# Kernel optimization log

Hardware: AMD Instinct MI355X
Metric: run time of the kernel (lower is better)

The kernel has to match this reference:

```python
import jax, jax.numpy as jnp
import numpy as np

B, IN_FEATURES, OUT_FEATURES, NUM_CONN, K_OPS = 512, 4096, 4096, 64, 4


def setup_inputs() -> dict:
    key = jax.random.key(0)
    k1, k2, k3 = jax.random.split(key, 3)
    x = jax.random.normal(k1, (B, IN_FEATURES), dtype=jnp.float32)
    # per-output random fan-in connections (randperm(in)[:num_conn] in original)
    connection_indices = jax.random.randint(k2, (OUT_FEATURES, NUM_CONN), 0, IN_FEATURES, dtype=jnp.int32)
    # per-output choice among the K aggregation operators
    operator_table_indices = jax.random.randint(k3, (OUT_FEATURES,), 0, K_OPS, dtype=jnp.int32)
    return {"x": x, "connection_indices": connection_indices,
            "operator_table_indices": operator_table_indices}


def reference(x, connection_indices, operator_table_indices):
    # gather: [B, out_features, num_connections]
    features = x[:, connection_indices]
    # operator_table = [mean, sum, amax, amin], each reducing dim=2
    # stacked along axis=1 -> output: [B, K, out_features]
    output = jnp.stack([
        features.mean(axis=2),
        features.sum(axis=2),
        features.max(axis=2),
        features.min(axis=2),
    ], axis=1)
    # select chosen operator per output unit -> fwd: [B, out_features]
    idx = operator_table_indices[None, None, :]  # [1,1,O] broadcast over batch
    fwd = jnp.take_along_axis(output, idx, axis=1)[:, 0, :]
    return (fwd, output)
```

## Files before the change

### kernel.cpp

```cpp
#include <hip/hip_runtime.h>

#define IN_F   4096
#define OUT_F  4096
#define BATCH  512
#define NCONN  64
#define BT     4
#define OGRP   1024
#define NTHR   1024

typedef _Float16 h4v __attribute__((ext_vector_type(4)));

__global__ __launch_bounds__(256) void connT_kernel(const int* __restrict__ conn,
                                                    int* __restrict__ connT) {
    __shared__ int tile[64][65];
    const int o0 = blockIdx.x * 64;
    const int tx = threadIdx.x & 63;
    const int ty = threadIdx.x >> 6;
#pragma unroll
    for (int r = 0; r < 16; ++r) {
        const int row = ty * 16 + r;
        tile[row][tx] = conn[(size_t)(o0 + row) * NCONN + tx];
    }
    __syncthreads();
#pragma unroll
    for (int r = 0; r < 16; ++r) {
        const int k = ty * 16 + r;
        connT[(size_t)k * OUT_F + o0 + tx] = tile[tx][k];
    }
}

__global__ __launch_bounds__(NTHR, 8) void agg_kernel(const float* __restrict__ x,
                                                      const int* __restrict__ connT,
                                                      const int* __restrict__ opidx,
                                                      float* __restrict__ out) {
    __shared__ alignas(16) _Float16 xs[IN_F * BT];

    const int bid   = blockIdx.x;
    const int btile = (bid & 7) * 16 + (bid >> 5);
    const int og    = (bid >> 3) & 3;
    const int o0    = og * OGRP;
    const int b0    = btile * BT;
    const int t     = threadIdx.x;

    const int bb   = t & 3;
    const int joff = t >> 2;
    const float* __restrict__ xrow = x + (size_t)(b0 + bb) * IN_F;
#pragma unroll 4
    for (int it = 0; it < 16; ++it) {
        const int j = it * 256 + joff;
        xs[j * BT + bb] = (_Float16)xrow[j];
    }
    __syncthreads();

    const int o = o0 + t;
    const int* __restrict__ cp = connT + o;

    float s0 = 0.f, s1 = 0.f, s2 = 0.f, s3 = 0.f;
    float mx0 = -__builtin_inff(), mx1 = mx0, mx2 = mx0, mx3 = mx0;
    float mn0 =  __builtin_inff(), mn1 = mn0, mn2 = mn0, mn3 = mn0;

    int idx[8];
#pragma unroll
    for (int q = 0; q < 8; ++q) idx[q] = cp[(size_t)q * OUT_F];

    for (int kb = 0; kb < NCONN; kb += 8) {
        h4v v[8];
#pragma unroll
        for (int q = 0; q < 8; ++q)
            v[q] = *reinterpret_cast<const h4v*>(&xs[idx[q] * BT]);
        if (kb + 8 < NCONN) {
#pragma unroll
            for (int q = 0; q < 8; ++q) idx[q] = cp[(size_t)(kb + 8 + q) * OUT_F];
        }
#pragma unroll
        for (int q = 0; q < 8; ++q) {
            const float f0 = (float)v[q][0];
            const float f1 = (float)v[q][1];
            const float f2 = (float)v[q][2];
            const float f3 = (float)v[q][3];
            s0 += f0;  s1 += f1;  s2 += f2;  s3 += f3;
            mx0 = fmaxf(mx0, f0); mx1 = fmaxf(mx1, f1);
            mx2 = fmaxf(mx2, f2); mx3 = fmaxf(mx3, f3);
            mn0 = fminf(mn0, f0); mn1 = fminf(mn1, f1);
            mn2 = fminf(mn2, f2); mn3 = fminf(mn3, f3);
        }
    }

    const int op = opidx[o];
    float* __restrict__ fwd  = out;
    float* __restrict__ outp = out + (size_t)BATCH * OUT_F;

    const float sv[4] = {s0, s1, s2, s3};
    const float xv[4] = {mx0, mx1, mx2, mx3};
    const float nv[4] = {mn0, mn1, mn2, mn3};
#pragma unroll
    for (int i = 0; i < 4; ++i) {
        const float ss = sv[i];
        const float mm = ss * 0.015625f;
        const float hx = xv[i];
        const float ln = nv[i];
        const float fw = (op == 0) ? mm : (op == 1) ? ss : (op == 2) ? hx : ln;
        const size_t rowO = (size_t)(b0 + i) * (4 * OUT_F) + o;
        __builtin_nontemporal_store(fw, fwd + (size_t)(b0 + i) * OUT_F + o);
        __builtin_nontemporal_store(mm, outp + rowO);
        __builtin_nontemporal_store(ss, outp + rowO + OUT_F);
        __builtin_nontemporal_store(hx, outp + rowO + 2 * OUT_F);
        __builtin_nontemporal_store(ln, outp + rowO + 3 * OUT_F);
    }
}

extern "C" void kernel_launch(void* const* d_in, const int* in_sizes, int n_in,
                              void* d_out, int out_size, void* d_ws, size_t ws_size,
                              hipStream_t stream) {
    const float* x     = (const float*)d_in[0];
    const int*   conn  = (const int*)d_in[1];
    const int*   opidx = (const int*)d_in[2];
    float*       out   = (float*)d_out;
    int*         connT = (int*)d_ws;

    connT_kernel<<<OUT_F / 64, 256, 0, stream>>>(conn, connT);

    const int nblocks = (BATCH / BT) * (OUT_F / OGRP);
    agg_kernel<<<nblocks, NTHR, 0, stream>>>(x, connT, opidx, out);
}
```

Before: 27.97 us.

## Pack connection indices as u16x4 and do max/min in packed half precision

The preprocessing kernel now packs connection indices into 16-bit values grouped four per 8-byte vector. The aggregation kernel can then load four indices per global access, with a two-stage register prefetch. Max and min are now computed on packed fp16 vectors instead of after converting each element to fp32, which cuts VALU work; sums stay in fp32. This relies on IN_F fitting in 16 bits. Max/min results are unchanged, since the inputs were already rounded to fp16.

```diff
diff --git a/kernel.cpp b/kernel.cpp
--- a/kernel.cpp
+++ b/kernel.cpp
@@ -8,29 +8,56 @@
 #define OGRP   1024
 #define NTHR   1024
 
+typedef unsigned short u16;
+typedef u16 us4 __attribute__((ext_vector_type(4)));
 typedef _Float16 h4v __attribute__((ext_vector_type(4)));
 
-__global__ __launch_bounds__(256) void connT_kernel(const int* __restrict__ conn,
-                                                    int* __restrict__ connT) {
-    __shared__ int tile[64][65];
+static __device__ __forceinline__ h4v h4_max(h4v a, h4v b) {
+    h4v r;
+#pragma unroll
+    for (int i = 0; i < 4; ++i) r[i] = a[i] > b[i] ? a[i] : b[i];
+    return r;
+}
+static __device__ __forceinline__ h4v h4_min(h4v a, h4v b) {
+    h4v r;
+#pragma unroll
+    for (int i = 0; i < 4; ++i) r[i] = a[i] < b[i] ? a[i] : b[i];
+    return r;
+}
+
+__global__ __launch_bounds__(256) void pack_kernel(const int* __restrict__ conn,
+                                                   us4* __restrict__ connP) {
+    __shared__ u16 tile[64][68];
     const int o0 = blockIdx.x * 64;
-    const int tx = threadIdx.x & 63;
-    const int ty = threadIdx.x >> 6;
+    const int t  = threadIdx.x;
+    const int ol = t >> 2;
+    const int4* __restrict__ c4 = reinterpret_cast<const int4*>(conn);
 #pragma unroll
-    for (int r = 0; r < 16; ++r) {
-        const int row = ty * 16 + r;
-        tile[row][tx] = conn[(size_t)(o0 + row) * NCONN + tx];
+    for (int i = 0; i < 4; ++i) {
+        const int4 v = c4[(size_t)(o0 + ol) * 16 + (t & 3) * 4 + i];
+        const int kbase = (t & 3) * 16 + i * 4;
+        tile[ol][kbase + 0] = (u16)v.x;
+        tile[ol][kbase + 1] = (u16)v.y;
+        tile[ol][kbase + 2] = (u16)v.z;
+        tile[ol][kbase + 3] = (u16)v.w;
     }
     __syncthreads();
+    const int o  = o0 + (t & 63);
+    const int k0 = (t >> 6) * 4;
 #pragma unroll
-    for (int r = 0; r < 16; ++r) {
-        const int k = ty * 16 + r;
-        connT[(size_t)k * OUT_F + o0 + tx] = tile[tx][k];
+    for (int i = 0; i < 4; ++i) {
+        const int kb = k0 + i;
+        us4 p;
+        p[0] = tile[t & 63][4 * kb + 0];
+        p[1] = tile[t & 63][4 * kb + 1];
+        p[2] = tile[t & 63][4 * kb + 2];
+        p[3] = tile[t & 63][4 * kb + 3];
+        connP[(size_t)kb * OUT_F + o] = p;
     }
 }
 
 __global__ __launch_bounds__(NTHR, 8) void agg_kernel(const float* __restrict__ x,
-                                                      const int* __restrict__ connT,
+                                                      const us4* __restrict__ connP,
                                                       const int* __restrict__ opidx,
                                                       float* __restrict__ out) {
     __shared__ alignas(16) _Float16 xs[IN_F * BT];
@@ -53,59 +80,67 @@
     __syncthreads();
 
     const int o = o0 + t;
-    const int* __restrict__ cp = connT + o;
+    const us4* __restrict__ cp = connP + o;
+
+    us4 i0 = cp[0];
+    us4 i1 = cp[OUT_F];
+    us4 i2 = cp[2 * (size_t)OUT_F];
+    us4 i3 = cp[3 * (size_t)OUT_F];
 
     float s0 = 0.f, s1 = 0.f, s2 = 0.f, s3 = 0.f;
-    float mx0 = -__builtin_inff(), mx1 = mx0, mx2 = mx0, mx3 = mx0;
-    float mn0 =  __builtin_inff(), mn1 = mn0, mn2 = mn0, mn3 = mn0;
+    const _Float16 HNEG = __builtin_bit_cast(_Float16, (u16)0xFC00);
+    const _Float16 HPOS = __builtin_bit_cast(_Float16, (u16)0x7C00);
+    h4v hx = {HNEG, HNEG, HNEG, HNEG};
+    h4v hn = {HPOS, HPOS, HPOS, HPOS};
 
-    int idx[8];
-#pragma unroll
-    for (int q = 0; q < 8; ++q) idx[q] = cp[(size_t)q * OUT_F];
+    const h4v* __restrict__ xs4 = reinterpret_cast<const h4v*>(xs);
 
-    for (int kb = 0; kb < NCONN; kb += 8) {
-        h4v v[8];
-#pragma unroll
-        for (int q = 0; q < 8; ++q)
-            v[q] = *reinterpret_cast<const h4v*>(&xs[idx[q] * BT]);
-        if (kb + 8 < NCONN) {
-#pragma unroll
-            for (int q = 0; q < 8; ++q) idx[q] = cp[(size_t)(kb + 8 + q) * OUT_F];
+    for (int kb = 0; kb < 16; kb += 2) {
+        h4v g[8];
+        g[0] = xs4[i0[0]];  g[1] = xs4[i0[1]];
+        g[2] = xs4[i0[2]];  g[3] = xs4[i0[3]];
+        g[4] = xs4[i1[0]];  g[5] = xs4[i1[1]];
+        g[6] = xs4[i1[2]];  g[7] = xs4[i1[3]];
+
+        us4 inA = i2, inB = i3;
+        if (kb < 12) {
+            inA = cp[(size_t)(kb + 4) * OUT_F];
+            inB = cp[(size_t)(kb + 5) * OUT_F];
         }
+
 #pragma unroll
         for (int q = 0; q < 8; ++q) {
-            const float f0 = (float)v[q][0];
-            const float f1 = (float)v[q][1];
-            const float f2 = (float)v[q][2];
-            const float f3 = (float)v[q][3];
-            s0 += f0;  s1 += f1;  s2 += f2;  s3 += f3;
-            mx0 = fmaxf(mx0, f0); mx1 = fmaxf(mx1, f1);
-            mx2 = fmaxf(mx2, f2); mx3 = fmaxf(mx3, f3);
-            mn0 = fminf(mn0, f0); mn1 = fminf(mn1, f1);
-            mn2 = fminf(mn2, f2); mn3 = fminf(mn3, f3);
+            hx = h4_max(hx, g[q]);
+            hn = h4_min(hn, g[q]);
+            s0 += (float)g[q][0];
+            s1 += (float)g[q][1];
+            s2 += (float)g[q][2];
+            s3 += (float)g[q][3];
         }
+        i0 = i2; i1 = i3; i2 = inA; i3 = inB;
     }
+
+    const float sv[4] = {s0, s1, s2, s3};
+    const float xv[4] = {(float)hx[0], (float)hx[1], (float)hx[2], (float)hx[3]};
+    const float nv[4] = {(float)hn[0], (float)hn[1], (float)hn[2], (float)hn[3]};
 
     const int op = opidx[o];
     float* __restrict__ fwd  = out;
     float* __restrict__ outp = out + (size_t)BATCH * OUT_F;
 
-    const float sv[4] = {s0, s1, s2, s3};
-    const float xv[4] = {mx0, mx1, mx2, mx3};
-    const float nv[4] = {mn0, mn1, mn2, mn3};
 #pragma unroll
     for (int i = 0; i < 4; ++i) {
         const float ss = sv[i];
         const float mm = ss * 0.015625f;
-        const float hx = xv[i];
-        const float ln = nv[i];
-        const float fw = (op == 0) ? mm : (op == 1) ? ss : (op == 2) ? hx : ln;
+        const float hxv = xv[i];
+        const float lnv = nv[i];
+        const float fw = (op == 0) ? mm : (op == 1) ? ss : (op == 2) ? hxv : lnv;
         const size_t rowO = (size_t)(b0 + i) * (4 * OUT_F) + o;
         __builtin_nontemporal_store(fw, fwd + (size_t)(b0 + i) * OUT_F + o);
         __builtin_nontemporal_store(mm, outp + rowO);
         __builtin_nontemporal_store(ss, outp + rowO + OUT_F);
-        __builtin_nontemporal_store(hx, outp + rowO + 2 * OUT_F);
-        __builtin_nontemporal_store(ln, outp + rowO + 3 * OUT_F);
+        __builtin_nontemporal_store(hxv, outp + rowO + 2 * OUT_F);
+        __builtin_nontemporal_store(lnv, outp + rowO + 3 * OUT_F);
     }
 }
 
@@ -116,10 +151,10 @@
     const int*   conn  = (const int*)d_in[1];
     const int*   opidx = (const int*)d_in[2];
     float*       out   = (float*)d_out;
-    int*         connT = (int*)d_ws;
+    us4*         connP = (us4*)d_ws;
 
-    connT_kernel<<<OUT_F / 64, 256, 0, stream>>>(conn, connT);
+    pack_kernel<<<OUT_F / 64, 256, 0, stream>>>(conn, connP);
 
     const int nblocks = (BATCH / BT) * (OUT_F / OGRP);
-    agg_kernel<<<nblocks, NTHR, 0, stream>>>(x, connT, opidx, out);
+    agg_kernel<<<nblocks, NTHR, 0, stream>>>(x, connP, opidx, out);
 }
```

New measurement: 38.44 us. +37.5%, slower.

## Split gathers between LDS and a transposed fp16 global copy, packed half min/max

Applied to the files above, without the earlier changes.

Adds a transpose kernel that writes x as a [IN_F, BATCH] fp16 array, so each gather of four batch values becomes one 8-byte global load. In the aggregation kernel, alternating wavefronts take half of their 64 connections from the LDS tile and half from this global copy, in opposite order, to spread the load between the LDS and the vector memory path. Max and min now run as packed fp16 vector operations instead of scalar fp32. The cost is an extra kernel launch and a full pass over x, more global traffic, and some added code complexity.

```diff
diff --git a/kernel.cpp b/kernel.cpp
--- a/kernel.cpp
+++ b/kernel.cpp
@@ -8,7 +8,39 @@
 #define OGRP   1024
 #define NTHR   1024
 
+typedef unsigned short u16;
 typedef _Float16 h4v __attribute__((ext_vector_type(4)));
+
+__global__ __launch_bounds__(256) void transpose_kernel(const float* __restrict__ x,
+                                                        _Float16* __restrict__ xTh) {
+    __shared__ float tile[64 * 68];
+    const int j0 = blockIdx.x * 64;
+    const int b0 = blockIdx.y * 64;
+    const int t  = threadIdx.x;
+    const int c  = t & 15;
+    const int r0 = t >> 4;
+#pragma unroll
+    for (int it = 0; it < 4; ++it) {
+        const int r  = r0 + it * 16;
+        const int pc = (4 * c) ^ (((r >> 2) & 7) << 2);
+        const float4 v = *reinterpret_cast<const float4*>(
+            x + (size_t)(b0 + r) * IN_F + j0 + 4 * c);
+        *reinterpret_cast<float4*>(&tile[r * 68 + pc]) = v;
+    }
+    __syncthreads();
+#pragma unroll
+    for (int it = 0; it < 4; ++it) {
+        const int jj = r0 + it * 16;
+        h4v v;
+#pragma unroll
+        for (int i = 0; i < 4; ++i) {
+            const int rr   = 4 * c + i;
+            const int pcol = jj ^ (((rr >> 2) & 7) << 2);
+            v[i] = (_Float16)tile[rr * 68 + pcol];
+        }
+        *reinterpret_cast<h4v*>(xTh + (size_t)(j0 + jj) * BATCH + b0 + 4 * c) = v;
+    }
+}
 
 __global__ __launch_bounds__(256) void connT_kernel(const int* __restrict__ conn,
                                                     int* __restrict__ connT) {
@@ -30,6 +62,7 @@
 }
 
 __global__ __launch_bounds__(NTHR, 8) void agg_kernel(const float* __restrict__ x,
+                                                      const _Float16* __restrict__ xTh,
                                                       const int* __restrict__ connT,
                                                       const int* __restrict__ opidx,
                                                       float* __restrict__ out) {
@@ -54,58 +87,87 @@
 
     const int o = o0 + t;
     const int* __restrict__ cp = connT + o;
+    const h4v* __restrict__ xs4 = reinterpret_cast<const h4v*>(xs);
+    const h4v* __restrict__ xg  = reinterpret_cast<const h4v*>(xTh) + (b0 >> 2);
 
     float s0 = 0.f, s1 = 0.f, s2 = 0.f, s3 = 0.f;
-    float mx0 = -__builtin_inff(), mx1 = mx0, mx2 = mx0, mx3 = mx0;
-    float mn0 =  __builtin_inff(), mn1 = mn0, mn2 = mn0, mn3 = mn0;
+    const _Float16 HNEG = __builtin_bit_cast(_Float16, (u16)0xFC00);
+    const _Float16 HPOS = __builtin_bit_cast(_Float16, (u16)0x7C00);
+    h4v hx = {HNEG, HNEG, HNEG, HNEG};
+    h4v hn = {HPOS, HPOS, HPOS, HPOS};
 
-    int idx[8];
+#define CONSUME(gq)                                                         \
+    do {                                                                    \
+        hx = __builtin_elementwise_max(hx, (gq));                           \
+        hn = __builtin_elementwise_min(hn, (gq));                           \
+        s0 = fmaf((float)(gq)[0], 1.0f, s0);                                \
+        s1 = fmaf((float)(gq)[1], 1.0f, s1);                                \
+        s2 = fmaf((float)(gq)[2], 1.0f, s2);                                \
+        s3 = fmaf((float)(gq)[3], 1.0f, s3);                                \
+    } while (0)
+
+    auto lds_phase = [&](int k0) {
+        int idx[8];
 #pragma unroll
-    for (int q = 0; q < 8; ++q) idx[q] = cp[(size_t)q * OUT_F];
+        for (int q = 0; q < 8; ++q) idx[q] = cp[(size_t)(k0 + q) * OUT_F];
+        for (int kb = 0; kb < 32; kb += 8) {
+            h4v g[8];
+#pragma unroll
+            for (int q = 0; q < 8; ++q) g[q] = xs4[idx[q]];
+            if (kb + 8 < 32) {
+#pragma unroll
+                for (int q = 0; q < 8; ++q)
+                    idx[q] = cp[(size_t)(k0 + kb + 8 + q) * OUT_F];
+            }
+#pragma unroll
+            for (int q = 0; q < 8; ++q) CONSUME(g[q]);
+        }
+    };
 
-    for (int kb = 0; kb < NCONN; kb += 8) {
-        h4v v[8];
+    auto glob_phase = [&](int k0) {
+        int idx[8];
 #pragma unroll
-        for (int q = 0; q < 8; ++q)
-            v[q] = *reinterpret_cast<const h4v*>(&xs[idx[q] * BT]);
-        if (kb + 8 < NCONN) {
+        for (int q = 0; q < 8; ++q) idx[q] = cp[(size_t)(k0 + q) * OUT_F];
+        for (int kb = 0; kb < 32; kb += 8) {
+            h4v g[8];
 #pragma unroll
-            for (int q = 0; q < 8; ++q) idx[q] = cp[(size_t)(kb + 8 + q) * OUT_F];
+            for (int q = 0; q < 8; ++q)
+                g[q] = xg[(size_t)idx[q] * (BATCH / 4)];
+            if (kb + 8 < 32) {
+#pragma unroll
+                for (int q = 0; q < 8; ++q)
+                    idx[q] = cp[(size_t)(k0 + kb + 8 + q) * OUT_F];
+            }
+#pragma unroll
+            for (int q = 0; q < 8; ++q) CONSUME(g[q]);
         }
-#pragma unroll
-        for (int q = 0; q < 8; ++q) {
-            const float f0 = (float)v[q][0];
-            const float f1 = (float)v[q][1];
-            const float f2 = (float)v[q][2];
-            const float f3 = (float)v[q][3];
-            s0 += f0;  s1 += f1;  s2 += f2;  s3 += f3;
-            mx0 = fmaxf(mx0, f0); mx1 = fmaxf(mx1, f1);
-            mx2 = fmaxf(mx2, f2); mx3 = fmaxf(mx3, f3);
-            mn0 = fminf(mn0, f0); mn1 = fminf(mn1, f1);
-            mn2 = fminf(mn2, f2); mn3 = fminf(mn3, f3);
-        }
-    }
+    };
+
+    if ((t >> 6) & 1) { lds_phase(0);  glob_phase(32); }
+    else              { glob_phase(0); lds_phase(32);  }
+#undef CONSUME
+
+    const float sv[4] = {s0, s1, s2, s3};
+    const float xv[4] = {(float)hx[0], (float)hx[1], (float)hx[2], (float)hx[3]};
+    const float nv[4] = {(float)hn[0], (float)hn[1], (float)hn[2], (float)hn[3]};
 
     const int op = opidx[o];
     float* __restrict__ fwd  = out;
     float* __restrict__ outp = out + (size_t)BATCH * OUT_F;
 
-    const float sv[4] = {s0, s1, s2, s3};
-    const float xv[4] = {mx0, mx1, mx2, mx3};
-    const float nv[4] = {mn0, mn1, mn2, mn3};
 #pragma unroll
     for (int i = 0; i < 4; ++i) {
         const float ss = sv[i];
         const float mm = ss * 0.015625f;
-        const float hx = xv[i];
-        const float ln = nv[i];
-        const float fw = (op == 0) ? mm : (op == 1) ? ss : (op == 2) ? hx : ln;
+        const float hxv = xv[i];
+        const float lnv = nv[i];
+        const float fw = (op == 0) ? mm : (op == 1) ? ss : (op == 2) ? hxv : lnv;
         const size_t rowO = (size_t)(b0 + i) * (4 * OUT_F) + o;
         __builtin_nontemporal_store(fw, fwd + (size_t)(b0 + i) * OUT_F + o);
         __builtin_nontemporal_store(mm, outp + rowO);
         __builtin_nontemporal_store(ss, outp + rowO + OUT_F);
-        __builtin_nontemporal_store(hx, outp + rowO + 2 * OUT_F);
-        __builtin_nontemporal_store(ln, outp + rowO + 3 * OUT_F);
+        __builtin_nontemporal_store(hxv, outp + rowO + 2 * OUT_F);
+        __builtin_nontemporal_store(lnv, outp + rowO + 3 * OUT_F);
     }
 }
 
@@ -116,10 +178,13 @@
     const int*   conn  = (const int*)d_in[1];
     const int*   opidx = (const int*)d_in[2];
     float*       out   = (float*)d_out;
-    int*         connT = (int*)d_ws;
+    _Float16*    xTh   = (_Float16*)d_ws;
+    int*         connT = (int*)((char*)d_ws + (size_t)IN_F * BATCH * 2);
 
     connT_kernel<<<OUT_F / 64, 256, 0, stream>>>(conn, connT);
+    dim3 tg(IN_F / 64, BATCH / 64);
+    transpose_kernel<<<tg, 256, 0, stream>>>(x, xTh);
 
     const int nblocks = (BATCH / BT) * (OUT_F / OGRP);
-    agg_kernel<<<nblocks, NTHR, 0, stream>>>(x, connT, opidx, out);
+    agg_kernel<<<nblocks, NTHR, 0, stream>>>(x, xTh, connT, opidx, out);
 }
```

Measured after the change: 92.92 us. +232.3%, slower.
